# Optimization experiments

Hardware: AMD Instinct MI355X
Metric: run time of the kernel (lower is better)

The kernel has to match this reference:

```python
import jax, jax.numpy as jnp
import numpy as np

NUM_EMB = 1024
EMB_DIM = 256
COMMITMENT_COST = 0.25


def setup_inputs() -> dict:
    key = jax.random.key(0)
    k1, k2 = jax.random.split(key)
    inp = jax.random.normal(k1, (64, EMB_DIM, 32, 32), dtype=jnp.float32)  # [B, C, H, W]
    emb_weight = jax.random.uniform(
        k2, (NUM_EMB, EMB_DIM), minval=-1.0 / NUM_EMB, maxval=1.0 / NUM_EMB, dtype=jnp.float32
    )
    return {"inp": inp, "emb_weight": emb_weight}


def reference(inp, emb_weight):
    sg = jax.lax.stop_gradient
    x = jnp.transpose(inp, (0, 2, 3, 1))              # [B, H, W, C]
    flat = x.reshape(-1, EMB_DIM)                      # [N, C]
    d = (jnp.sum(flat * flat, axis=1, keepdims=True)
         + jnp.sum(emb_weight * emb_weight, axis=1)
         - 2.0 * (flat @ emb_weight.T))
    idx = jnp.argmin(d, axis=1)                        # [N]
    encodings = jax.nn.one_hot(idx, NUM_EMB, dtype=jnp.float32)  # [N, K]
    e = emb_weight[idx].reshape(x.shape)               # [B, H, W, C]
    loss = jnp.mean((e - sg(x)) ** 2) + COMMITMENT_COST * jnp.mean((sg(e) - x) ** 2)
    e_ste = x + sg(e - x)                              # straight-through estimator
    avg_probs = jnp.mean(encodings, axis=0)
    perplexity = jnp.exp(-jnp.sum(avg_probs * jnp.log(avg_probs + 1e-10)))
    out = jnp.transpose(e_ste, (0, 3, 1, 2))           # back to [B, C, H, W]
    return loss, out, perplexity, encodings
```

## Files before the change

kernel.cpp:

```cpp
#include <hip/hip_runtime.h>
#include <hip/hip_bf16.h>
#include <math.h>
#include <float.h>

#define BB    64
#define CCH   256
#define KKE   1024
#define HWN   1024
#define NTOT  (BB*HWN)
#define OUT_ELE (BB*CCH*HWN)
#define LOSS_OFF 0
#define OUT_OFF  1
#define PERP_OFF (1 + OUT_ELE)
#define ENC_OFF  (2 + OUT_ELE)

#define WS_IDX    0
#define WS_ANORM  262144
#define WS_HIST   524288
#define WS_BNORM  528384
#define WS_MISC   532480
#define WS_LIST   536576
#define WS_EMBT   798720
#define WS_EHI    1847296
#define WS_ELO    2371584
#define WS_CD1    2895872
#define WS_CK1    4993024
#define WS_CD2    7090176

typedef __attribute__((ext_vector_type(4))) float f32x4;
typedef __attribute__((ext_vector_type(8))) short s16x8;

#define TAU 2e-4f
#define APAD 36

__device__ inline void merge_cand(float& d1, int& k1, float& d2,
                                  float od1, int ok1, float od2) {
    bool w = (od1 < d1) || (od1 == d1 && ok1 < k1);
    float loser_d1 = w ? d1 : od1;
    float winner_d2 = w ? od2 : d2;
    d2 = fminf(winner_d2, loser_d1);
    if (w) { d1 = od1; k1 = ok1; }
}

__global__ __launch_bounds__(256) void prep_kernel(const float* __restrict__ emb,
                                                   float* __restrict__ embT,
                                                   float* __restrict__ bnorm,
                                                   short* __restrict__ ehi,
                                                   short* __restrict__ elo,
                                                   unsigned int* __restrict__ hist,
                                                   float* __restrict__ misc) {
    const int k = blockIdx.x;
    const int t = threadIdx.x;
    float v = emb[k*CCH + t];
    embT[(size_t)t*KKE + k] = v;
    __hip_bfloat16 h = __float2bfloat16(v);
    float hf = __bfloat162float(h);
    __hip_bfloat16 l = __float2bfloat16(v - hf);
    size_t eoff = (size_t)(t >> 5)*32768 + (size_t)k*32 + (t & 31);
    ehi[eoff] = *(short*)&h;
    elo[eoff] = *(short*)&l;
    double sq = (double)v * (double)v;
    #pragma unroll
    for (int off = 32; off; off >>= 1) sq += __shfl_down(sq, off);
    __shared__ double wred[4];
    const int wave = t >> 6, lane = t & 63;
    if (lane == 0) wred[wave] = sq;
    __syncthreads();
    if (t == 0) bnorm[k] = (float)(wred[0] + wred[1] + wred[2] + wred[3]);
    if (blockIdx.x < 4) hist[blockIdx.x*256 + t] = 0u;
    if (blockIdx.x == 4 && t == 0) { misc[0] = 0.0f; ((int*)misc)[1] = 0; }
}

__global__ __launch_bounds__(256) void anorm_kernel(const float* __restrict__ inp,
                                                    float* __restrict__ anorm) {
    const int b  = blockIdx.y;
    const int hw = blockIdx.x * 256 + threadIdx.x;
    const float* p = inp + (size_t)b*CCH*HWN + hw;
    double s = 0.0;
    #pragma unroll 8
    for (int c = 0; c < CCH; ++c) {
        float v = p[(size_t)c*HWN];
        s += (double)v * (double)v;
    }
    anorm[b*HWN + hw] = (float)s;
}

__global__ __launch_bounds__(256, 3) void argmin_mfma(const float* __restrict__ inp,
                                                      const short* __restrict__ ehi,
                                                      const short* __restrict__ elo,
                                                      const float* __restrict__ anorm,
                                                      const float* __restrict__ bnorm,
                                                      float* __restrict__ cd1,
                                                      int* __restrict__ ck1,
                                                      float* __restrict__ cd2) {
    __shared__ short Ahi[128*APAD];
    __shared__ short Alo[128*APAD];
    __shared__ short Bhi[128*APAD];
    __shared__ short Blo[128*APAD];
    __shared__ float m_d1[2][128];
    __shared__ float m_d2[2][128];
    __shared__ int   m_k1[2][128];

    const int t    = threadIdx.x;
    const int w    = t >> 6;
    const int lane = t & 63;
    const int q    = lane >> 4;
    const int l15  = lane & 15;
    const int wn   = (w & 1) * 64;
    const int wkh  = w >> 1;
    const int wk   = wkh * 64;
    const int n0   = blockIdx.x * 128;
    const int k0   = blockIdx.y * 128;
    const int b    = n0 >> 10;
    const int hw0  = n0 & 1023;
    const float* gA = inp + (size_t)b*CCH*HWN + hw0;

    const int na = t & 127;
    const int ch = t >> 7;
    const int br = t >> 2;
    const int bc = (t & 3) * 8;

    f32x4 acc[4][4];
    #pragma unroll
    for (int i = 0; i < 4; ++i)
        #pragma unroll
        for (int j = 0; j < 4; ++j) acc[i][j] = (f32x4){0.f,0.f,0.f,0.f};

    for (int chunk = 0; chunk < 8; ++chunk) {
        const int c0 = chunk * 32;
        __syncthreads();
        float v[16];
        #pragma unroll
        for (int cc = 0; cc < 16; ++cc)
            v[cc] = gA[(size_t)(c0 + ch*16 + cc) * HWN + na];
        short hs[16], ls[16];
        #pragma unroll
        for (int cc = 0; cc < 16; ++cc) {
            __hip_bfloat16 h = __float2bfloat16(v[cc]);
            float hf = __bfloat162float(h);
            __hip_bfloat16 l = __float2bfloat16(v[cc] - hf);
            hs[cc] = *(short*)&h; ls[cc] = *(short*)&l;
        }
        *(s16x8*)&Ahi[na*APAD + ch*16]     = *(s16x8*)&hs[0];
        *(s16x8*)&Ahi[na*APAD + ch*16 + 8] = *(s16x8*)&hs[8];
        *(s16x8*)&Alo[na*APAD + ch*16]     = *(s16x8*)&ls[0];
        *(s16x8*)&Alo[na*APAD + ch*16 + 8] = *(s16x8*)&ls[8];
        {
            const size_t ebase = (size_t)chunk*32768 + (size_t)k0*32;
            *(s16x8*)&Bhi[br*APAD + bc]      = *(const s16x8*)&ehi[ebase + t*8];
            *(s16x8*)&Bhi[(64+br)*APAD + bc] = *(const s16x8*)&ehi[ebase + 2048 + t*8];
            *(s16x8*)&Blo[br*APAD + bc]      = *(const s16x8*)&elo[ebase + t*8];
            *(s16x8*)&Blo[(64+br)*APAD + bc] = *(const s16x8*)&elo[ebase + 2048 + t*8];
        }
        __syncthreads();
        s16x8 ah[4], al[4];
        #pragma unroll
        for (int rg = 0; rg < 4; ++rg) {
            ah[rg] = *(s16x8*)&Ahi[(wn + rg*16 + l15)*APAD + q*8];
            al[rg] = *(s16x8*)&Alo[(wn + rg*16 + l15)*APAD + q*8];
        }
        #pragma unroll
        for (int ct = 0; ct < 4; ++ct) {
            s16x8 bh = *(s16x8*)&Bhi[(wk + ct*16 + l15)*APAD + q*8];
            s16x8 bl = *(s16x8*)&Blo[(wk + ct*16 + l15)*APAD + q*8];
            #pragma unroll
            for (int rg = 0; rg < 4; ++rg) {
                acc[rg][ct] = __builtin_amdgcn_mfma_f32_16x16x32_bf16(ah[rg], bh, acc[rg][ct], 0, 0, 0);
                acc[rg][ct] = __builtin_amdgcn_mfma_f32_16x16x32_bf16(ah[rg], bl, acc[rg][ct], 0, 0, 0);
                acc[rg][ct] = __builtin_amdgcn_mfma_f32_16x16x32_bf16(al[rg], bh, acc[rg][ct], 0, 0, 0);
            }
        }
    }

    float bnv[4];
    #pragma unroll
    for (int ct = 0; ct < 4; ++ct) bnv[ct] = bnorm[k0 + wk + ct*16 + l15];

    #pragma unroll
    for (int rg = 0; rg < 4; ++rg) {
        #pragma unroll
        for (int reg = 0; reg < 4; ++reg) {
            const int nl = wn + rg*16 + q*4 + reg;
            const float a = anorm[n0 + nl];
            float d1 = FLT_MAX, d2 = FLT_MAX; int k1 = 0;
            #pragma unroll
            for (int ct = 0; ct < 4; ++ct) {
                float s = a + bnv[ct];
                float d = s - 2.0f * acc[rg][ct][reg];
                int   k = k0 + wk + ct*16 + l15;
                if (d < d1 || (d == d1 && k < k1)) { d2 = d1; d1 = d; k1 = k; }
                else d2 = fminf(d2, d);
            }
            #pragma unroll
            for (int off = 1; off < 16; off <<= 1) {
                float od1 = __shfl_xor(d1, off);
                int   ok1 = __shfl_xor(k1, off);
                float od2 = __shfl_xor(d2, off);
                merge_cand(d1, k1, d2, od1, ok1, od2);
            }
            if (l15 == 0) {
                m_d1[wkh][nl] = d1; m_k1[wkh][nl] = k1; m_d2[wkh][nl] = d2;
            }
        }
    }
    __syncthreads();
    if (t < 128) {
        float d1 = m_d1[0][t]; int k1 = m_k1[0][t]; float d2 = m_d2[0][t];
        merge_cand(d1, k1, d2, m_d1[1][t], m_k1[1][t], m_d2[1][t]);
        const size_t o = (size_t)blockIdx.y*NTOT + n0 + t;
        cd1[o] = d1; ck1[o] = k1; cd2[o] = d2;
    }
}

__global__ __launch_bounds__(256) void reduce_kernel(const float* __restrict__ cd1,
                                                     const int* __restrict__ ck1,
                                                     const float* __restrict__ cd2,
                                                     int* __restrict__ idx,
                                                     int* __restrict__ list,
                                                     int* __restrict__ counter) {
    const int n = blockIdx.x*256 + threadIdx.x;
    float d1 = cd1[n]; int k1 = ck1[n]; float d2 = cd2[n];
    #pragma unroll
    for (int kb = 1; kb < 8; ++kb) {
        const size_t o = (size_t)kb*NTOT + n;
        merge_cand(d1, k1, d2, cd1[o], ck1[o], cd2[o]);
    }
    idx[n] = k1;
    if (d2 - d1 < TAU) {
        int p = atomicAdd(counter, 1);
        list[p] = n;
    }
}

__global__ __launch_bounds__(256) void rescore_kernel(const float* __restrict__ inp,
                                                      const float* __restrict__ embT,
                                                      const float* __restrict__ anorm,
                                                      const float* __restrict__ bnorm,
                                                      const int* __restrict__ list,
                                                      const int* __restrict__ counter,
                                                      int* __restrict__ idx) {
    __shared__ float xs[256];
    __shared__ float rd[256];
    __shared__ int   rk[256];
    const int t = threadIdx.x;
    const int cnt = *counter;
    for (int f = blockIdx.x; f < cnt; f += gridDim.x) {
        const int n = list[f];
        const int b = n >> 10, hw = n & 1023;
        __syncthreads();
        xs[t] = inp[(size_t)b*CCH*HWN + (size_t)t*HWN + hw];
        __syncthreads();
        float dot0 = 0.f, dot1 = 0.f, dot2 = 0.f, dot3 = 0.f;
        #pragma unroll 4
        for (int c = 0; c < CCH; ++c) {
            const float xc = xs[c];
            const float* row = embT + (size_t)c*KKE + t;
            dot0 += xc * row[0];
            dot1 += xc * row[256];
            dot2 += xc * row[512];
            dot3 += xc * row[768];
        }
        const float a = anorm[n];
        float bd = FLT_MAX; int bk = 0;
        float dots[4] = {dot0, dot1, dot2, dot3};
        #pragma unroll
        for (int kk = 0; kk < 4; ++kk) {
            const int k = kk*256 + t;
            float s = a + bnorm[k];
            float d = s - 2.0f * dots[kk];
            if (d < bd || (d == bd && k < bk)) { bd = d; bk = k; }
        }
        rd[t] = bd; rk[t] = bk;
        __syncthreads();
        for (int stride = 128; stride; stride >>= 1) {
            if (t < stride) {
                float od = rd[t+stride]; int ok = rk[t+stride];
                if (od < rd[t] || (od == rd[t] && ok < rk[t])) { rd[t] = od; rk[t] = ok; }
            }
            __syncthreads();
        }
        if (t == 0) idx[n] = rk[0];
    }
}

__global__ __launch_bounds__(256) void onehot_kernel(const int* __restrict__ idx,
                                                     float* __restrict__ enc,
                                                     unsigned int* __restrict__ hist) {
    const int t = threadIdx.x;
    const int j4 = t * 4;
    for (int r = 0; r < 16; ++r) {
        const int n = blockIdx.x*16 + r;
        const int k = idx[n];
        float2 v0 = {0.0f, 0.0f}, v1 = {0.0f, 0.0f};
        if (k == j4)     v0.x = 1.0f;
        if (k == j4 + 1) v0.y = 1.0f;
        if (k == j4 + 2) v1.x = 1.0f;
        if (k == j4 + 3) v1.y = 1.0f;
        float* row = enc + (size_t)n * KKE;
        *(float2*)&row[j4]     = v0;
        *(float2*)&row[j4 + 2] = v1;
        if (t == 0) atomicAdd(&hist[k], 1u);
    }
}

__global__ __launch_bounds__(256) void out_loss_kernel(const float* __restrict__ inp,
                                                       const float* __restrict__ embT,
                                                       const int* __restrict__ idx,
                                                       float* __restrict__ out,
                                                       float* __restrict__ lossacc) {
    const int t = threadIdx.x;
    const size_t stride = (size_t)gridDim.x * 256;
    float lsum = 0.0f;
    for (size_t m = (size_t)blockIdx.x * 256 + t; m < (size_t)OUT_ELE; m += stride) {
        int hw = (int)(m & 1023);
        int c  = (int)((m >> 10) & 255);
        int b  = (int)(m >> 18);
        int k  = idx[b*HWN + hw];
        float e = embT[(size_t)c*KKE + k];
        float x = inp[m];
        out[m] = e;
        float df = e - x;
        lsum += df * df;
    }
    #pragma unroll
    for (int off = 32; off; off >>= 1) lsum += __shfl_down(lsum, off);
    __shared__ float wred[4];
    const int wave = t >> 6, lane = t & 63;
    if (lane == 0) wred[wave] = lsum;
    __syncthreads();
    if (t == 0) atomicAdd(lossacc, wred[0] + wred[1] + wred[2] + wred[3]);
}

__global__ __launch_bounds__(1024) void final_kernel(const unsigned int* __restrict__ hist,
                                                     const float* __restrict__ lossacc,
                                                     float* __restrict__ d_out) {
    const int t = threadIdx.x;
    float p = (float)hist[t] * (1.0f / 65536.0f);
    float v = p * logf(p + 1e-10f);
    #pragma unroll
    for (int off = 32; off; off >>= 1) v += __shfl_down(v, off);
    __shared__ float wred[16];
    const int wave = t >> 6, lane = t & 63;
    if (lane == 0) wred[wave] = v;
    __syncthreads();
    if (t == 0) {
        float s = 0.0f;
        #pragma unroll
        for (int i = 0; i < 16; ++i) s += wred[i];
        d_out[PERP_OFF] = expf(-s);
        d_out[LOSS_OFF] = 1.25f * (*lossacc) * (1.0f / (float)OUT_ELE);
    }
}

extern "C" void kernel_launch(void* const* d_in, const int* in_sizes, int n_in,
                              void* d_out, int out_size, void* d_ws, size_t ws_size,
                              hipStream_t stream) {
    (void)in_sizes; (void)n_in; (void)out_size; (void)ws_size;
    const float* inp = (const float*)d_in[0];
    const float* emb = (const float*)d_in[1];
    float* out = (float*)d_out;
    char* ws = (char*)d_ws;
    int*          idx     = (int*)(ws + WS_IDX);
    float*        anorm   = (float*)(ws + WS_ANORM);
    unsigned int* hist    = (unsigned int*)(ws + WS_HIST);
    float*        bnorm   = (float*)(ws + WS_BNORM);
    float*        misc    = (float*)(ws + WS_MISC);
    int*          list    = (int*)(ws + WS_LIST);
    float*        embT    = (float*)(ws + WS_EMBT);
    short*        ehi     = (short*)(ws + WS_EHI);
    short*        elo     = (short*)(ws + WS_ELO);
    float*        cd1     = (float*)(ws + WS_CD1);
    int*          ck1     = (int*)(ws + WS_CK1);
    float*        cd2     = (float*)(ws + WS_CD2);
    int*          counter = ((int*)misc) + 1;

    prep_kernel<<<dim3(KKE), dim3(256), 0, stream>>>(emb, embT, bnorm, ehi, elo, hist, misc);
    anorm_kernel<<<dim3(4, BB), dim3(256), 0, stream>>>(inp, anorm);
    argmin_mfma<<<dim3(512, 8), dim3(256), 0, stream>>>(inp, ehi, elo, anorm, bnorm, cd1, ck1, cd2);
    reduce_kernel<<<dim3(256), dim3(256), 0, stream>>>(cd1, ck1, cd2, idx, list, counter);
    rescore_kernel<<<dim3(512), dim3(256), 0, stream>>>(inp, embT, anorm, bnorm, list, counter, idx);
    onehot_kernel<<<dim3(4096), dim3(256), 0, stream>>>(idx, out + ENC_OFF, hist);
    out_loss_kernel<<<dim3(4096), dim3(256), 0, stream>>>(inp, embT, idx, out + OUT_OFF, misc);
    final_kernel<<<dim3(1), dim3(1024), 0, stream>>>(hist, misc, out);
}
```

Baseline: 761.6 us.

## Pre-split activations to bf16 hi/lo in MFMA fragment layout, load via global_load_lds

A new split kernel fuses the activation norm computation with converting the input into bf16 hi/lo pairs, stored in a per-lane MFMA fragment layout in workspace. The embedding split uses the same fragment layout, so the argmin GEMM can stream both operands straight into LDS with global_load_lds and read each fragment with one contiguous vector load. Before, every one of the 8 k-blocks re-read and re-split the fp32 input. The grid is swapped so that k-tiles sharing an n-tile run next to each other, which should improve L2 reuse, and occupancy is raised to 4. In exchange the change writes and reads an extra 64 MB of split activations in workspace.

New measurement: 766.2 us. Within noise of the previous version (+0.6%).

```diff
diff --git a/kernel.cpp b/kernel.cpp
--- a/kernel.cpp
+++ b/kernel.cpp
@@ -26,12 +26,17 @@
 #define WS_CD1    2895872
 #define WS_CK1    4993024
 #define WS_CD2    7090176
+#define WS_AHI    16777216
+#define WS_ALO    50331648
 
 typedef __attribute__((ext_vector_type(4))) float f32x4;
 typedef __attribute__((ext_vector_type(8))) short s16x8;
 
 #define TAU 2e-4f
-#define APAD 36
+
+#define GLOAD_LDS(gptr, ldsptr) \
+    __builtin_amdgcn_global_load_lds((const __attribute__((address_space(1))) unsigned int*)(gptr), \
+                                     (__attribute__((address_space(3))) unsigned int*)(ldsptr), 16, 0, 0)
 
 __device__ inline void merge_cand(float& d1, int& k1, float& d2,
                                   float od1, int ok1, float od2) {
@@ -56,36 +61,83 @@
     __hip_bfloat16 h = __float2bfloat16(v);
     float hf = __bfloat162float(h);
     __hip_bfloat16 l = __float2bfloat16(v - hf);
-    size_t eoff = (size_t)(t >> 5)*32768 + (size_t)k*32 + (t & 31);
+    const int chunk = t >> 5;
+    const int lane  = (k & 15) | (((t >> 3) & 3) << 4);
+    const size_t eoff = ((size_t)(chunk*64 + (k >> 4))*64 + lane)*8 + (t & 7);
     ehi[eoff] = *(short*)&h;
     elo[eoff] = *(short*)&l;
     double sq = (double)v * (double)v;
     #pragma unroll
     for (int off = 32; off; off >>= 1) sq += __shfl_down(sq, off);
     __shared__ double wred[4];
-    const int wave = t >> 6, lane = t & 63;
-    if (lane == 0) wred[wave] = sq;
+    const int wave = t >> 6, ln = t & 63;
+    if (ln == 0) wred[wave] = sq;
     __syncthreads();
     if (t == 0) bnorm[k] = (float)(wred[0] + wred[1] + wred[2] + wred[3]);
     if (blockIdx.x < 4) hist[blockIdx.x*256 + t] = 0u;
     if (blockIdx.x == 4 && t == 0) { misc[0] = 0.0f; ((int*)misc)[1] = 0; }
 }
 
-__global__ __launch_bounds__(256) void anorm_kernel(const float* __restrict__ inp,
+__global__ __launch_bounds__(256) void split_kernel(const float* __restrict__ inp,
+                                                    short* __restrict__ ahi,
+                                                    short* __restrict__ alo,
                                                     float* __restrict__ anorm) {
-    const int b  = blockIdx.y;
-    const int hw = blockIdx.x * 256 + threadIdx.x;
-    const float* p = inp + (size_t)b*CCH*HWN + hw;
-    double s = 0.0;
-    #pragma unroll 8
-    for (int c = 0; c < CCH; ++c) {
-        float v = p[(size_t)c*HWN];
-        s += (double)v * (double)v;
-    }
-    anorm[b*HWN + hw] = (float)s;
-}
-
-__global__ __launch_bounds__(256, 3) void argmin_mfma(const float* __restrict__ inp,
+    __shared__ float xs[256][32];
+    __shared__ double dred[8][32];
+    const int t = threadIdx.x;
+    const int n0 = blockIdx.x * 32;
+    const int b = n0 >> 10;
+    const int hw0 = n0 & 1023;
+    const float* src = inp + (size_t)b*CCH*HWN + hw0;
+    const int n4 = (t & 7) * 4, cl = t >> 3;
+    #pragma unroll
+    for (int c0 = 0; c0 < CCH; c0 += 32) {
+        float4 v = *(const float4*)&src[(size_t)(c0 + cl)*HWN + n4];
+        *(float4*)&xs[c0 + cl][n4] = v;
+    }
+    __syncthreads();
+    {
+        const int nl = t & 31, part = t >> 5;
+        double s = 0.0;
+        #pragma unroll 8
+        for (int c = 0; c < 32; ++c) {
+            float v = xs[part*32 + c][nl];
+            s += (double)v * (double)v;
+        }
+        dred[part][nl] = s;
+    }
+    __syncthreads();
+    if (t < 32) {
+        double s = 0.0;
+        #pragma unroll
+        for (int p = 0; p < 8; ++p) s += dred[p][t];
+        anorm[n0 + t] = (float)s;
+    }
+    const int ntg0 = n0 >> 4;
+    #pragma unroll
+    for (int i = 0; i < 4; ++i) {
+        const int s = t + 256*i;
+        const int chunk = s >> 7;
+        const int nt = (s >> 6) & 1;
+        const int lane = s & 63;
+        const int m = lane & 15, q = lane >> 4;
+        short hsv[8], lsv[8];
+        #pragma unroll
+        for (int j = 0; j < 8; ++j) {
+            float v = xs[chunk*32 + q*8 + j][nt*16 + m];
+            __hip_bfloat16 h = __float2bfloat16(v);
+            float hf = __bfloat162float(h);
+            __hip_bfloat16 l = __float2bfloat16(v - hf);
+            hsv[j] = *(short*)&h; lsv[j] = *(short*)&l;
+        }
+        const size_t off = ((size_t)(chunk*4096 + ntg0 + nt)*64 + lane)*8;
+        *(s16x8*)&ahi[off] = *(s16x8*)&hsv[0];
+        *(s16x8*)&alo[off] = *(s16x8*)&lsv[0];
+    }
+}
+
+__global__ __launch_bounds__(256, 4) void argmin_mfma(const short* __restrict__ ahi,
+                                                      const short* __restrict__ alo,
                                                       const short* __restrict__ ehi,
                                                       const short* __restrict__ elo,
                                                       const float* __restrict__ anorm,
@@ -93,10 +145,10 @@
                                                       float* __restrict__ cd1,
                                                       int* __restrict__ ck1,
                                                       float* __restrict__ cd2) {
-    __shared__ short Ahi[128*APAD];
-    __shared__ short Alo[128*APAD];
-    __shared__ short Bhi[128*APAD];
-    __shared__ short Blo[128*APAD];
+    __shared__ short Ah[8*512];
+    __shared__ short Al[8*512];
+    __shared__ short Bh[8*512];
+    __shared__ short Bl[8*512];
     __shared__ float m_d1[2][128];
     __shared__ float m_d2[2][128];
     __shared__ int   m_k1[2][128];
@@ -109,16 +161,10 @@
     const int wn   = (w & 1) * 64;
     const int wkh  = w >> 1;
     const int wk   = wkh * 64;
-    const int n0   = blockIdx.x * 128;
-    const int k0   = blockIdx.y * 128;
-    const int b    = n0 >> 10;
-    const int hw0  = n0 & 1023;
-    const float* gA = inp + (size_t)b*CCH*HWN + hw0;
-
-    const int na = t & 127;
-    const int ch = t >> 7;
-    const int br = t >> 2;
-    const int bc = (t & 3) * 8;
+    const int k0     = blockIdx.x * 128;
+    const int ktile0 = blockIdx.x * 8;
+    const int n0     = blockIdx.y * 128;
+    const int ntg0   = n0 >> 4;
 
     f32x4 acc[4][4];
     #pragma unroll
@@ -127,47 +173,41 @@
         for (int j = 0; j < 4; ++j) acc[i][j] = (f32x4){0.f,0.f,0.f,0.f};
 
     for (int chunk = 0; chunk < 8; ++chunk) {
-        const int c0 = chunk * 32;
         __syncthreads();
-        float v[16];
-        #pragma unroll
-        for (int cc = 0; cc < 16; ++cc)
-            v[cc] = gA[(size_t)(c0 + ch*16 + cc) * HWN + na];
-        short hs[16], ls[16];
-        #pragma unroll
-        for (int cc = 0; cc < 16; ++cc) {
-            __hip_bfloat16 h = __float2bfloat16(v[cc]);
-            float hf = __bfloat162float(h);
-            __hip_bfloat16 l = __float2bfloat16(v[cc] - hf);
-            hs[cc] = *(short*)&h; ls[cc] = *(short*)&l;
-        }
-        *(s16x8*)&Ahi[na*APAD + ch*16]     = *(s16x8*)&hs[0];
-        *(s16x8*)&Ahi[na*APAD + ch*16 + 8] = *(s16x8*)&hs[8];
-        *(s16x8*)&Alo[na*APAD + ch*16]     = *(s16x8*)&ls[0];
-        *(s16x8*)&Alo[na*APAD + ch*16 + 8] = *(s16x8*)&ls[8];
-        {
-            const size_t ebase = (size_t)chunk*32768 + (size_t)k0*32;
-            *(s16x8*)&Bhi[br*APAD + bc]      = *(const s16x8*)&ehi[ebase + t*8];
-            *(s16x8*)&Bhi[(64+br)*APAD + bc] = *(const s16x8*)&ehi[ebase + 2048 + t*8];
-            *(s16x8*)&Blo[br*APAD + bc]      = *(const s16x8*)&elo[ebase + t*8];
-            *(s16x8*)&Blo[(64+br)*APAD + bc] = *(const s16x8*)&elo[ebase + 2048 + t*8];
+        #pragma unroll
+        for (int i = 0; i < 4; ++i) {
+            const int sel = w*4 + i;
+            const int rt  = sel & 7;
+            const bool hi = (sel < 8);
+            {
+                const short* g = hi ? ahi : alo;
+                short* d = hi ? &Ah[rt*512] : &Al[rt*512];
+                GLOAD_LDS(g + ((size_t)(chunk*4096 + ntg0 + rt)*64 + lane)*8, d);
+            }
+            {
+                const short* g = hi ? ehi : elo;
+                short* d = hi ? &Bh[rt*512] : &Bl[rt*512];
+                GLOAD_LDS(g + ((size_t)(chunk*64 + ktile0 + rt)*64 + lane)*8, d);
+            }
         }
         __syncthreads();
-        s16x8 ah[4], al[4];
+        s16x8 ah4[4], al4[4];
         #pragma unroll
         for (int rg = 0; rg < 4; ++rg) {
-            ah[rg] = *(s16x8*)&Ahi[(wn + rg*16 + l15)*APAD + q*8];
-            al[rg] = *(s16x8*)&Alo[(wn + rg*16 + l15)*APAD + q*8];
+            const int nt = (w & 1)*4 + rg;
+            ah4[rg] = *(s16x8*)&Ah[nt*512 + lane*8];
+            al4[rg] = *(s16x8*)&Al[nt*512 + lane*8];
         }
         #pragma unroll
         for (int ct = 0; ct < 4; ++ct) {
-            s16x8 bh = *(s16x8*)&Bhi[(wk + ct*16 + l15)*APAD + q*8];
-            s16x8 bl = *(s16x8*)&Blo[(wk + ct*16 + l15)*APAD + q*8];
+            const int kt = wkh*4 + ct;
+            s16x8 bh = *(s16x8*)&Bh[kt*512 + lane*8];
+            s16x8 bl = *(s16x8*)&Bl[kt*512 + lane*8];
             #pragma unroll
             for (int rg = 0; rg < 4; ++rg) {
-                acc[rg][ct] = __builtin_amdgcn_mfma_f32_16x16x32_bf16(ah[rg], bh, acc[rg][ct], 0, 0, 0);
-                acc[rg][ct] = __builtin_amdgcn_mfma_f32_16x16x32_bf16(ah[rg], bl, acc[rg][ct], 0, 0, 0);
-                acc[rg][ct] = __builtin_amdgcn_mfma_f32_16x16x32_bf16(al[rg], bh, acc[rg][ct], 0, 0, 0);
+                acc[rg][ct] = __builtin_amdgcn_mfma_f32_16x16x32_bf16(ah4[rg], bh, acc[rg][ct], 0, 0, 0);
+                acc[rg][ct] = __builtin_amdgcn_mfma_f32_16x16x32_bf16(ah4[rg], bl, acc[rg][ct], 0, 0, 0);
+                acc[rg][ct] = __builtin_amdgcn_mfma_f32_16x16x32_bf16(al4[rg], bh, acc[rg][ct], 0, 0, 0);
             }
         }
     }
@@ -207,7 +247,7 @@
     if (t < 128) {
         float d1 = m_d1[0][t]; int k1 = m_k1[0][t]; float d2 = m_d2[0][t];
         merge_cand(d1, k1, d2, m_d1[1][t], m_k1[1][t], m_d2[1][t]);
-        const size_t o = (size_t)blockIdx.y*NTOT + n0 + t;
+        const size_t o = (size_t)blockIdx.x*NTOT + n0 + t;
         cd1[o] = d1; ck1[o] = k1; cd2[o] = d2;
     }
 }
@@ -372,11 +412,13 @@
     float*        cd1     = (float*)(ws + WS_CD1);
     int*          ck1     = (int*)(ws + WS_CK1);
     float*        cd2     = (float*)(ws + WS_CD2);
+    short*        ahi     = (short*)(ws + WS_AHI);
+    short*        alo     = (short*)(ws + WS_ALO);
     int*          counter = ((int*)misc) + 1;
 
     prep_kernel<<<dim3(KKE), dim3(256), 0, stream>>>(emb, embT, bnorm, ehi, elo, hist, misc);
-    anorm_kernel<<<dim3(4, BB), dim3(256), 0, stream>>>(inp, anorm);
-    argmin_mfma<<<dim3(512, 8), dim3(256), 0, stream>>>(inp, ehi, elo, anorm, bnorm, cd1, ck1, cd2);
+    split_kernel<<<dim3(2048), dim3(256), 0, stream>>>(inp, ahi, alo, anorm);
+    argmin_mfma<<<dim3(8, 512), dim3(256), 0, stream>>>(ahi, alo, ehi, elo, anorm, bnorm, cd1, ck1, cd2);
     reduce_kernel<<<dim3(256), dim3(256), 0, stream>>>(cd1, ck1, cd2, idx, list, counter);
     rescore_kernel<<<dim3(512), dim3(256), 0, stream>>>(inp, embT, anorm, bnorm, list, counter, idx);
     onehot_kernel<<<dim3(4096), dim3(256), 0, stream>>>(idx, out + ENC_OFF, hist);
```
